# Kernel optimization log

Hardware: AMD Instinct MI355X
Metric: run time of the kernel (lower is better)

The kernel has to match this reference:

```python
import jax, jax.numpy as jnp
import numpy as np

NUM_HEADS = 16
HEAD_DIM = 128
HIDDEN = 2048
C_KV = 512
C_Q = 1024
ROPE_DIM = 64
BATCH = 2
SEQ = 2048
ROPE_BASE = 10000.0


def _rope_cos_sin(seq_len, dim, dtype):
    # standard RoPE tables: [seq, dim] with concatenated (half, half) freqs
    inv_freq = 1.0 / (ROPE_BASE ** (jnp.arange(0, dim, 2, dtype=jnp.float32) / dim))
    t = jnp.arange(seq_len, dtype=jnp.float32)
    freqs = jnp.outer(t, inv_freq)                      # [S, dim/2]
    emb = jnp.concatenate([freqs, freqs], axis=-1)      # [S, dim]
    return jnp.cos(emb).astype(dtype), jnp.sin(emb).astype(dtype)


def _rotate_half(x):
    x1, x2 = jnp.split(x, 2, axis=-1)
    return jnp.concatenate([-x2, x1], axis=-1)


def _apply_rope(x, cos, sin):
    # x: [B, S, H, D]; cos/sin: [S, D] -> broadcast over batch and heads
    c = cos[None, :, None, :]
    s = sin[None, :, None, :]
    return x * c + _rotate_half(x) * s


def setup_inputs() -> dict:
    key = jax.random.key(0)
    ks = jax.random.split(key, 10)

    def xavier(k, shape):
        fan_in, fan_out = shape
        limit = np.sqrt(6.0 / (fan_in + fan_out))
        return jax.random.uniform(k, shape, jnp.float32, -limit, limit)

    hidden_states = jax.random.normal(ks[0], (BATCH, SEQ, HIDDEN), jnp.float32)
    # causal mask: 1 = masked out (positions j > i)
    causal = jnp.triu(jnp.ones((SEQ, SEQ), jnp.int32), k=1)
    mask = jnp.broadcast_to(causal[None, None], (BATCH, 1, SEQ, SEQ))
    return {
        "hidden_states": hidden_states,
        "mask": mask,
        "W_DKV": xavier(ks[1], (HIDDEN, C_KV)),
        "W_UK": xavier(ks[2], (C_KV, NUM_HEADS * HEAD_DIM)),
        "W_UV": xavier(ks[3], (C_KV, NUM_HEADS * HEAD_DIM)),
        "W_DQ": xavier(ks[4], (HIDDEN, C_Q)),
        "W_UQ": xavier(ks[5], (C_Q, NUM_HEADS * HEAD_DIM)),
        "W_QR": xavier(ks[6], (C_Q, NUM_HEADS * ROPE_DIM)),
        "W_KR": xavier(ks[7], (HIDDEN, ROPE_DIM)),
        "W_O": xavier(ks[8], (NUM_HEADS * HEAD_DIM, HIDDEN)),
    }


def reference(hidden_states, mask, W_DKV, W_UK, W_UV, W_DQ, W_UQ, W_QR, W_KR, W_O):
    B, S, _ = hidden_states.shape
    scale = 1.0 / jnp.sqrt(jnp.float32(HEAD_DIM + ROPE_DIM))

    c_KV = hidden_states @ W_DKV                         # [B,S,c_kv]
    k_C = (c_KV @ W_UK).reshape(B, S, NUM_HEADS, HEAD_DIM)
    v = (c_KV @ W_UV).reshape(B, S, NUM_HEADS, HEAD_DIM)
    c_Q = hidden_states @ W_DQ                           # [B,S,c_q]
    q_C = (c_Q @ W_UQ).reshape(B, S, NUM_HEADS, HEAD_DIM)
    q_R = (c_Q @ W_QR).reshape(B, S, NUM_HEADS, ROPE_DIM)
    k_R = (hidden_states @ W_KR).reshape(B, S, 1, ROPE_DIM)

    cos, sin = _rope_cos_sin(S, ROPE_DIM, hidden_states.dtype)
    q_R = _apply_rope(q_R, cos, sin)
    k_R = _apply_rope(k_R, cos, sin)
    k_R = jnp.broadcast_to(k_R, (B, S, NUM_HEADS, ROPE_DIM))

    q = jnp.concatenate([q_C, q_R], axis=-1)             # [B,S,H,D+R]
    k = jnp.concatenate([k_C, k_R], axis=-1)             # [B,S,H,D+R]

    scores = jnp.einsum('bqhd,bkhd->bhqk', q, k) * scale
    scores = scores + mask.astype(scores.dtype) * jnp.asarray(-1e9, scores.dtype)
    probs = jax.nn.softmax(scores, axis=-1)
    out = jnp.einsum('bhqk,bkhd->bqhd', probs, v).reshape(B, S, NUM_HEADS * HEAD_DIM)
    return out @ W_O
```

## Files before the change

kernel.cpp:

```cpp
#include <hip/hip_runtime.h>
#include <hip/hip_bf16.h>

typedef __bf16 bf16x8 __attribute__((ext_vector_type(8)));
typedef float f32x4 __attribute__((ext_vector_type(4)));
typedef float f32x16 __attribute__((ext_vector_type(16)));
using BF = __hip_bfloat16;

constexpr int B_   = 2;
constexpr int S_   = 2048;
constexpr int NH_  = 16;
constexpr int HD_  = 128;
constexpr int HID_ = 2048;
constexpr int CKV_ = 512;
constexpr int CQ_  = 1024;
constexpr int RD_  = 64;
constexpr int M_   = B_ * S_;
constexpr int DQK_ = HD_ + RD_;

__device__ __forceinline__ f32x4 mfma16(bf16x8 a, bf16x8 b, f32x4 c) {
  return __builtin_amdgcn_mfma_f32_16x16x32_bf16(a, b, c, 0, 0, 0);
}
__device__ __forceinline__ f32x16 mfma32(bf16x8 a, bf16x8 b, f32x16 c) {
  return __builtin_amdgcn_mfma_f32_32x32x16_bf16(a, b, c, 0, 0, 0);
}
__device__ __forceinline__ unsigned cvtpk(float a, float b) {
  unsigned r;
  asm("v_cvt_pk_bf16_f32 %0, %1, %2" : "=v"(r) : "v"(a), "v"(b));
  return r;
}
__device__ __forceinline__ void gload16(const void* g, void* lds) {
  __builtin_amdgcn_global_load_lds((const __attribute__((address_space(1))) void*)g,
                                   (__attribute__((address_space(3))) void*)lds,
                                   16, 0, 0);
}
__device__ __forceinline__ void plswap(unsigned& x, unsigned& y, bool hi) {
#if __has_builtin(__builtin_amdgcn_permlane32_swap)
  typedef unsigned u32x2 __attribute__((ext_vector_type(2)));
  u32x2 r = __builtin_amdgcn_permlane32_swap(x, y, false, false);
  x = r[0];
  y = r[1];
#else
  unsigned sx = (unsigned)__shfl_xor((int)x, 32, 64);
  unsigned sy = (unsigned)__shfl_xor((int)y, 32, 64);
  unsigned nx = hi ? sy : x;
  unsigned ny = hi ? y : sx;
  x = nx;
  y = ny;
#endif
}

__global__ __launch_bounds__(256) void f2b_kern(const float* __restrict__ in,
                                                BF* __restrict__ out, int n4) {
  int i = blockIdx.x * 256 + threadIdx.x;
  if (i >= n4) return;
  float4 v = reinterpret_cast<const float4*>(in)[i];
  BF o[4] = {__float2bfloat16(v.x), __float2bfloat16(v.y),
             __float2bfloat16(v.z), __float2bfloat16(v.w)};
  reinterpret_cast<uint2*>(out)[i] = *reinterpret_cast<uint2*>(o);
}

__global__ __launch_bounds__(256) void wtrans_all(const float* __restrict__ w0,
                                                  const float* __restrict__ w1,
                                                  const float* __restrict__ w2,
                                                  const float* __restrict__ w3,
                                                  const float* __restrict__ w4,
                                                  const float* __restrict__ w5,
                                                  const float* __restrict__ w6,
                                                  const float* __restrict__ w7,
                                                  BF* __restrict__ tCat1,
                                                  BF* __restrict__ tCat2,
                                                  BF* __restrict__ tCat3,
                                                  BF* __restrict__ tWO) {
  const int cum[9] = {0, 1024, 3072, 3328, 4352, 5376, 7424, 8448, 12544};
  const int nxt[8] = {16, 32, 4, 64, 64, 64, 32, 64};
  const int Kt[8]  = {2048, 2048, 2048, 512, 512, 1024, 1024, 2048};
  const int Nt[8]  = {512, 1024, 64, 2048, 2048, 2048, 1024, 2048};
  int bid = blockIdx.x;
  int j = 0;
#pragma unroll
  for (int t = 1; t < 8; t++)
    if (bid >= cum[t]) j = t;
  const float* in = (j == 0) ? w0 : (j == 1) ? w1 : (j == 2) ? w2 : (j == 3) ? w3
                   : (j == 4) ? w4 : (j == 5) ? w5 : (j == 6) ? w6 : w7;
  BF* out = (j == 0) ? tCat1 : (j == 1) ? tCat1 + (size_t)512 * 2048
           : (j == 2) ? tCat1 + (size_t)1536 * 2048
           : (j == 3) ? tCat2 : (j == 4) ? tCat2 + (size_t)2048 * 512
           : (j == 5) ? tCat3 : (j == 6) ? tCat3 + (size_t)2048 * 1024 : tWO;
  const int K = Kt[j], N = Nt[j];
  int rem = bid - cum[j];
  int bx = rem % nxt[j], by = rem / nxt[j];
  int n0 = bx * 32, k0 = by * 32;

  __shared__ float t[32][33];
  int tx = threadIdx.x, ty = threadIdx.y;
#pragma unroll
  for (int j4 = 0; j4 < 4; j4++) {
    int k = k0 + ty + j4 * 8, n = n0 + tx;
    t[ty + j4 * 8][tx] = (n < N) ? in[(size_t)k * N + n] : 0.f;
  }
  __syncthreads();
#pragma unroll
  for (int j4 = 0; j4 < 4; j4++) {
    int n = n0 + ty + j4 * 8, k = k0 + tx;
    out[(size_t)n * K + k] = __float2bfloat16(t[tx][ty + j4 * 8]);
  }
}

template <int F>
__global__ __launch_bounds__(256) void gemm_f(const BF* __restrict__ A,
                                              const BF* __restrict__ Bt,
                                              void* __restrict__ C0,
                                              void* __restrict__ C1,
                                              void* __restrict__ C2,
                                              int M, int N, int K) {
  __shared__ BF As[3][128][32];
  __shared__ BF Bs[3][128][32];
  const int tid = threadIdx.x;
  const int w = tid >> 6, l = tid & 63;
  const int lr = l & 15, lg = l >> 4;
  const int wr = w >> 1, wc = w & 1;
  const int gx = gridDim.x;
  const int nwg = gx * gridDim.y;
  const int f = blockIdx.y * gx + blockIdx.x;
  const int swz = (f & 7) * (nwg >> 3) + (f >> 3);
  const int m0 = (swz / gx) * 128, n0 = (swz % gx) * 128;

  f32x4 acc[4][4];
#pragma unroll
  for (int m = 0; m < 4; m++)
#pragma unroll
    for (int n = 0; n < 4; n++) acc[m][n] = (f32x4){0.f, 0.f, 0.f, 0.f};

  auto STAGE = [&](int buf, int k0) {
#pragma unroll
    for (int j = 0; j < 2; j++) {
      int idx = tid + j * 256;
      int row = idx >> 2, seg = idx & 3;
      gload16(A + (size_t)(m0 + row) * K + k0 + seg * 8, &As[buf][0][0] + idx * 8);
      gload16(Bt + (size_t)(n0 + row) * K + k0 + seg * 8, &Bs[buf][0][0] + idx * 8);
    }
  };

  const int nk = K >> 5;
  STAGE(0, 0);
  if (nk > 1) STAGE(1, 32);
  asm volatile("s_waitcnt vmcnt(4)" ::: "memory");
  __builtin_amdgcn_sched_barrier(0);
  __builtin_amdgcn_s_barrier();

  int cur = 0;
  for (int ki = 0; ki < nk; ki++) {
    bf16x8 af[4], bfr[4];
#pragma unroll
    for (int m = 0; m < 4; m++)
      af[m] = *reinterpret_cast<const bf16x8*>(&As[cur][wr * 64 + m * 16 + lr][lg * 8]);
#pragma unroll
    for (int n = 0; n < 4; n++)
      bfr[n] = *reinterpret_cast<const bf16x8*>(&Bs[cur][wc * 64 + n * 16 + lr][lg * 8]);
    if (ki + 2 < nk) {
      int nb = cur + 2; if (nb >= 3) nb -= 3;
      STAGE(nb, (ki + 2) << 5);
    }
    __builtin_amdgcn_sched_barrier(0);
    __builtin_amdgcn_s_setprio(1);
#pragma unroll
    for (int m = 0; m < 4; m++)
#pragma unroll
      for (int n = 0; n < 4; n++) acc[m][n] = mfma16(af[m], bfr[n], acc[m][n]);
    __builtin_amdgcn_s_setprio(0);
    __builtin_amdgcn_sched_barrier(0);
    if (ki + 1 < nk) {
      if (ki + 2 < nk) {
        asm volatile("s_waitcnt vmcnt(4)" ::: "memory");
      } else {
        asm volatile("s_waitcnt vmcnt(0)" ::: "memory");
      }
      __builtin_amdgcn_sched_barrier(0);
      __builtin_amdgcn_s_barrier();
    }
    cur = cur + 1; if (cur >= 3) cur = 0;
  }

#pragma unroll
  for (int m = 0; m < 4; m++) {
#pragma unroll
    for (int n = 0; n < 4; n++) {
#pragma unroll
      for (int j = 0; j < 4; j++) {
        int row = m0 + wr * 64 + m * 16 + lg * 4 + j;
        int col = n0 + wc * 64 + n * 16 + lr;
        float v = acc[m][n][j];
        if constexpr (F == 1) {
          if (col < 512)
            ((BF*)C0)[(size_t)row * 512 + col] = __float2bfloat16(v);
          else if (col < 1536)
            ((BF*)C1)[(size_t)row * 1024 + (col - 512)] = __float2bfloat16(v);
          else
            ((BF*)C2)[(size_t)row * 128 + (col - 1536)] = __float2bfloat16(v);
        } else {
          ((float*)C0)[(size_t)row * 2048 + col] = v;
        }
      }
    }
  }
}

__global__ __launch_bounds__(256) void gemm_f23(const BF* __restrict__ cQ,
                                                const BF* __restrict__ t3,
                                                BF* __restrict__ qbuf,
                                                BF* __restrict__ qRt,
                                                const BF* __restrict__ cKV,
                                                const BF* __restrict__ t2,
                                                BF* __restrict__ kbuf,
                                                BF* __restrict__ vTb) {
  __shared__ BF As[3][128][32];
  __shared__ BF Bs[3][128][32];
  const int tid = threadIdx.x;
  const int w = tid >> 6, l = tid & 63;
  const int lr = l & 15, lg = l >> 4;
  const int wr = w >> 1, wc = w & 1;
  const int f = blockIdx.y * 56 + blockIdx.x;
  const int swz = (f & 7) * (1792 >> 3) + (f >> 3);
  const int xt = swz % 56;
  const int m0 = (swz / 56) * 128;
  const bool isF3 = xt < 24;
  const BF* A  = isF3 ? cQ : cKV;
  const BF* Bt = isF3 ? t3 : t2;
  const int K  = isF3 ? 1024 : 512;
  const int n0 = (isF3 ? xt : xt - 24) * 128;

  f32x4 acc[4][4];
#pragma unroll
  for (int m = 0; m < 4; m++)
#pragma unroll
    for (int n = 0; n < 4; n++) acc[m][n] = (f32x4){0.f, 0.f, 0.f, 0.f};

  auto STAGE = [&](int buf, int k0) {
#pragma unroll
    for (int j = 0; j < 2; j++) {
      int idx = tid + j * 256;
      int row = idx >> 2, seg = idx & 3;
      gload16(A + (size_t)(m0 + row) * K + k0 + seg * 8, &As[buf][0][0] + idx * 8);
      gload16(Bt + (size_t)(n0 + row) * K + k0 + seg * 8, &Bs[buf][0][0] + idx * 8);
    }
  };

  const int nk = K >> 5;
  STAGE(0, 0);
  STAGE(1, 32);
  asm volatile("s_waitcnt vmcnt(4)" ::: "memory");
  __builtin_amdgcn_sched_barrier(0);
  __builtin_amdgcn_s_barrier();

  int cur = 0;
  for (int ki = 0; ki < nk; ki++) {
    bf16x8 af[4], bfr[4];
#pragma unroll
    for (int m = 0; m < 4; m++)
      af[m] = *reinterpret_cast<const bf16x8*>(&As[cur][wr * 64 + m * 16 + lr][lg * 8]);
#pragma unroll
    for (int n = 0; n < 4; n++)
      bfr[n] = *reinterpret_cast<const bf16x8*>(&Bs[cur][wc * 64 + n * 16 + lr][lg * 8]);
    if (ki + 2 < nk) {
      int nb = cur + 2; if (nb >= 3) nb -= 3;
      STAGE(nb, (ki + 2) << 5);
    }
    __builtin_amdgcn_sched_barrier(0);
    __builtin_amdgcn_s_setprio(1);
#pragma unroll
    for (int m = 0; m < 4; m++)
#pragma unroll
      for (int n = 0; n < 4; n++) acc[m][n] = mfma16(af[m], bfr[n], acc[m][n]);
    __builtin_amdgcn_s_setprio(0);
    __builtin_amdgcn_sched_barrier(0);
    if (ki + 1 < nk) {
      if (ki + 2 < nk) {
        asm volatile("s_waitcnt vmcnt(4)" ::: "memory");
      } else {
        asm volatile("s_waitcnt vmcnt(0)" ::: "memory");
      }
      __builtin_amdgcn_sched_barrier(0);
      __builtin_amdgcn_s_barrier();
    }
    cur = cur + 1; if (cur >= 3) cur = 0;
  }

#pragma unroll
  for (int m = 0; m < 4; m++) {
#pragma unroll
    for (int n = 0; n < 4; n++) {
#pragma unroll
      for (int j = 0; j < 4; j++) {
        int row = m0 + wr * 64 + m * 16 + lg * 4 + j;
        int col = n0 + wc * 64 + n * 16 + lr;
        float v = acc[m][n][j];
        int b = row >> 11, s = row & 2047;
        if (isF3) {
          if (col < 2048) {
            int h = col >> 7, d = col & 127;
            qbuf[((size_t)(b * 16 + h) * 2048 + s) * 192 + d] = __float2bfloat16(v);
          } else {
            qRt[(size_t)row * 1024 + (col - 2048)] = __float2bfloat16(v);
          }
        } else {
          if (col < 2048) {
            int h = col >> 7, d = col & 127;
            kbuf[((size_t)(b * 16 + h) * 2048 + s) * 192 + d] = __float2bfloat16(v);
          } else {
            int c2 = col - 2048, h = c2 >> 7, d = c2 & 127;
            vTb[((size_t)(b * 16 + h) * 128 + d) * 2048 + s] = __float2bfloat16(v);
          }
        }
      }
    }
  }
}

__global__ __launch_bounds__(256) void rope_q(const BF* __restrict__ qr, BF* __restrict__ qb) {
  int idx = blockIdx.x * 256 + threadIdx.x;
  int d = idx & 63, h = (idx >> 6) & 15, m = idx >> 10;
  int s = m & 2047, b = m >> 11;
  float x = __bfloat162float(qr[(size_t)(m << 10) + (h << 6) + d]);
  float other = __bfloat162float(qr[(size_t)(m << 10) + (h << 6) + (d ^ 32)]);
  float rot = (d < 32) ? -other : other;
  int di = d & 31;
  float arg = (float)s * powf(10000.f, -(float)di / 32.0f);
  float c = cosf(arg), sn = sinf(arg);
  qb[((size_t)(b * 16 + h) * 2048 + s) * 192 + 128 + d] = __float2bfloat16(x * c + rot * sn);
}

__global__ __launch_bounds__(256) void rope_k(const BF* __restrict__ kr, BF* __restrict__ kb) {
  int idx = blockIdx.x * 256 + threadIdx.x;
  int d = idx & 63, m = idx >> 6;
  int s = m & 2047, b = m >> 11;
  float x = __bfloat162float(kr[(size_t)m * 128 + d]);
  float other = __bfloat162float(kr[(size_t)m * 128 + (d ^ 32)]);
  float rot = (d < 32) ? -other : other;
  int di = d & 31;
  float arg = (float)s * powf(10000.f, -(float)di / 32.0f);
  float val = x * cosf(arg) + rot * sinf(arg);
  BF v = __float2bfloat16(val);
#pragma unroll
  for (int h = 0; h < 16; h++)
    kb[((size_t)(b * 16 + h) * 2048 + s) * 192 + 128 + d] = v;
}

__global__ __launch_bounds__(256, 2) void attn_kern(const BF* __restrict__ qb,
                                                    const BF* __restrict__ kb,
                                                    const BF* __restrict__ vT,
                                                    BF* __restrict__ o) {
  const int yy = blockIdx.y;
  const bool second = yy >= 16;
  const int bh = second ? ((yy - 16) * 2 + 1) : (yy * 2);
  const int qt = second ? (int)blockIdx.x : (15 - (int)blockIdx.x);
  const int q0 = qt * 128;
  const int tid = threadIdx.x;
  const int w = tid >> 6, l = tid & 63;
  const int lo5 = l & 31;
  const int hi = l >> 5;
  const int l7 = l & 7;

  __shared__ __align__(16) char smem[81920];

  const int q = q0 + w * 32 + lo5;
  const int qmax = q0 + w * 32 + 31;

  bf16x8 aq[12];
  {
    const BF* qrow = qb + ((size_t)bh * 2048 + q) * 192;
#pragma unroll
    for (int kst = 0; kst < 12; kst++)
      aq[kst] = *reinterpret_cast<const bf16x8*>(qrow + kst * 16 + hi * 8);
  }

  f32x16 Oacc[4];
#pragma unroll
  for (int dt = 0; dt < 4; dt++)
#pragma unroll
    for (int r = 0; r < 16; r++) Oacc[dt][r] = 0.f;
  float mrow = -3e38f, lrow = 0.f;

  const float scale = 0.07216878364870323f;
  const int nch = (q0 + 128) >> 6;

  auto STAGE = [&](int buf, int ch) {
    const int cc = ch << 6;
    BF* Ks = (BF*)(smem + buf * 40960);
    BF* Vs = (BF*)(smem + buf * 40960 + 24576);
#pragma unroll
    for (int j2 = 0; j2 < 6; j2++) {
      int D = tid + j2 * 256;
      int row = D / 24, sp = D % 24;
      int sl = sp ^ (row & 7);
      gload16(kb + ((size_t)bh * 2048 + cc + row) * 192 + sl * 8, Ks + D * 8);
    }
#pragma unroll
    for (int j2 = 0; j2 < 4; j2++) {
      int D = tid + j2 * 256;
      int row = D >> 3, sp = D & 7;
      int sl = sp ^ (row & 7);
      gload16(vT + ((size_t)bh * 128 + row) * 2048 + cc + sl * 8, Vs + D * 8);
    }
  };

  STAGE(0, 0);
  __syncthreads();

  for (int ch = 0; ch < nch; ch++) {
    const int c0 = ch << 6;
    const int cur = ch & 1;
    if (ch + 1 < nch) STAGE(cur ^ 1, ch + 1);
    __builtin_amdgcn_sched_barrier(0);
    BF* Ks = (BF*)(smem + cur * 40960);
    BF* Vs = (BF*)(smem + cur * 40960 + 24576);

    f32x16 sf[2];
    __builtin_amdgcn_s_setprio(1);
#pragma unroll
    for (int t = 0; t < 2; t++) {
      if (c0 + t * 32 <= qmax) {
        f32x16 a0, a1;
#pragma unroll
        for (int r = 0; r < 16; r++) { a0[r] = 0.f; a1[r] = 0.f; }
#pragma unroll
        for (int kst = 0; kst < 12; kst++) {
          bf16x8 kfr = *reinterpret_cast<const bf16x8*>(
              Ks + (t * 32 + lo5) * 192 + (((kst * 2 + hi) ^ l7) * 8));
          if (kst & 1) a1 = mfma32(kfr, aq[kst], a1);
          else         a0 = mfma32(kfr, aq[kst], a0);
        }
        sf[t] = a0 + a1;
      } else {
#pragma unroll
        for (int r = 0; r < 16; r++) sf[t][r] = 0.f;
      }
    }
    __builtin_amdgcn_s_setprio(0);

    float mx = -3e38f;
#pragma unroll
    for (int t = 0; t < 2; t++) {
#pragma unroll
      for (int r = 0; r < 16; r++) {
        int key = c0 + t * 32 + (r & 3) + 8 * (r >> 2) + 4 * hi;
        float v = sf[t][r] * scale;
        v = (key <= q) ? v : -1e30f;
        sf[t][r] = v;
        mx = fmaxf(mx, v);
      }
    }
    mx = fmaxf(mx, __shfl_xor(mx, 32, 64));
    float mnew = fmaxf(mrow, mx);
    float corr = __expf(mrow - mnew);
    mrow = mnew;
    float psum = 0.f;
#pragma unroll
    for (int t = 0; t < 2; t++)
#pragma unroll
      for (int r = 0; r < 16; r++) {
        float p = __expf(sf[t][r] - mnew);
        sf[t][r] = p;
        psum += p;
      }
    psum += __shfl_xor(psum, 32, 64);
    lrow = lrow * corr + psum;
#pragma unroll
    for (int dt = 0; dt < 4; dt++) Oacc[dt] *= corr;

    bf16x8 pb[4];
#pragma unroll
    for (int ks = 0; ks < 4; ks++) {
      if (c0 + ks * 16 > qmax) continue;
      int t = ks >> 1, base = (ks & 1) * 8;
      unsigned Xa = cvtpk(sf[t][base + 0], sf[t][base + 1]);
      unsigned Xb = cvtpk(sf[t][base + 2], sf[t][base + 3]);
      unsigned Ya = cvtpk(sf[t][base + 4], sf[t][base + 5]);
      unsigned Yb = cvtpk(sf[t][base + 6], sf[t][base + 7]);
      plswap(Xa, Ya, hi != 0);
      plswap(Xb, Yb, hi != 0);
      union { unsigned u[4]; bf16x8 v; } pk_;
      pk_.u[0] = Xa; pk_.u[1] = Xb; pk_.u[2] = Ya; pk_.u[3] = Yb;
      pb[ks] = pk_.v;
    }

    __builtin_amdgcn_s_setprio(1);
#pragma unroll
    for (int ks = 0; ks < 4; ks++) {
      if (c0 + ks * 16 > qmax) continue;
#pragma unroll
      for (int dt = 0; dt < 4; dt++) {
        bf16x8 vfr = *reinterpret_cast<const bf16x8*>(
            Vs + (dt * 32 + lo5) * 64 + (((ks * 2 + hi) ^ l7) * 8));
        Oacc[dt] = mfma32(vfr, pb[ks], Oacc[dt]);
      }
    }
    __builtin_amdgcn_s_setprio(0);
    __syncthreads();
  }

  BF* Osh = (BF*)smem;
  float rinv = 1.0f / lrow;
  const int orow = w * 32 + lo5;
#pragma unroll
  for (int dt = 0; dt < 4; dt++) {
#pragma unroll
    for (int g = 0; g < 4; g++) {
      unsigned d0 = cvtpk(Oacc[dt][g * 4 + 0] * rinv, Oacc[dt][g * 4 + 1] * rinv);
      unsigned d1 = cvtpk(Oacc[dt][g * 4 + 2] * rinv, Oacc[dt][g * 4 + 3] * rinv);
      uint2 pr; pr.x = d0; pr.y = d1;
      *reinterpret_cast<uint2*>(Osh + orow * 136 + dt * 32 + g * 8 + hi * 4) = pr;
    }
  }
  __syncthreads();
  const int b = bh >> 4, h = bh & 15;
  const int cb = tid & 15, rb = tid >> 4;
#pragma unroll
  for (int rr = 0; rr < 8; rr++) {
    int row = rb + rr * 16;
    bf16x8 v = *reinterpret_cast<const bf16x8*>(Osh + row * 136 + cb * 8);
    *reinterpret_cast<bf16x8*>(o + ((size_t)(b * 2048 + q0 + row)) * 2048 + h * 128 + cb * 8) = v;
  }
}

extern "C" void kernel_launch(void* const* d_in, const int* in_sizes, int n_in,
                              void* d_out, int out_size, void* d_ws, size_t ws_size,
                              hipStream_t stream) {
  const float* hs   = (const float*)d_in[0];
  const float* wDKV = (const float*)d_in[2];
  const float* wUK  = (const float*)d_in[3];
  const float* wUV  = (const float*)d_in[4];
  const float* wDQ  = (const float*)d_in[5];
  const float* wUQ  = (const float*)d_in[6];
  const float* wQR  = (const float*)d_in[7];
  const float* wKR  = (const float*)d_in[8];
  const float* wO   = (const float*)d_in[9];
  float* out = (float*)d_out;

  char* ws = (char*)d_ws;
  size_t off = 0;
  auto alloc = [&](size_t bytes) -> char* {
    char* p = ws + off;
    off += (bytes + 255) & ~(size_t)255;
    return p;
  };
  BF* hsb   = (BF*)alloc((size_t)M_ * HID_ * 2);
  BF* tCat1 = (BF*)alloc((size_t)1664 * HID_ * 2);
  BF* tCat2 = (BF*)alloc((size_t)4096 * CKV_ * 2);
  BF* tCat3 = (BF*)alloc((size_t)3072 * CQ_ * 2);
  BF* tWO   = (BF*)alloc((size_t)HID_ * (NH_*HD_) * 2);
  BF* cKV   = (BF*)alloc((size_t)M_ * CKV_ * 2);
  BF* cQ    = (BF*)alloc((size_t)M_ * CQ_ * 2);
  BF* qbuf  = (BF*)alloc((size_t)B_ * NH_ * S_ * DQK_ * 2);
  BF* kbuf  = (BF*)alloc((size_t)B_ * NH_ * S_ * DQK_ * 2);
  BF* vTb   = (BF*)alloc((size_t)B_ * NH_ * HD_ * S_ * 2);
  BF* qRt   = (BF*)alloc((size_t)M_ * (NH_*RD_) * 2);
  BF* kRt   = (BF*)alloc((size_t)M_ * 128 * 2);
  BF* aout  = (BF*)alloc((size_t)M_ * (NH_*HD_) * 2);

  f2b_kern<<<(M_ * HID_ / 4 + 255) / 256, 256, 0, stream>>>(hs, hsb, M_ * HID_ / 4);

  wtrans_all<<<12544, dim3(32, 8), 0, stream>>>(wDKV, wDQ, wKR, wUK, wUV, wUQ, wQR, wO,
                                                tCat1, tCat2, tCat3, tWO);

  gemm_f<1><<<dim3(1664 / 128, M_ / 128), 256, 0, stream>>>(hsb, tCat1, cKV, cQ, kRt, M_, 1664, HID_);
  gemm_f23<<<dim3(56, M_ / 128), 256, 0, stream>>>(cQ, tCat3, qbuf, qRt, cKV, tCat2, kbuf, vTb);

  rope_q<<<(M_ * NH_ * RD_) / 256, 256, 0, stream>>>(qRt, qbuf);
  rope_k<<<(M_ * RD_) / 256, 256, 0, stream>>>(kRt, kbuf);

  attn_kern<<<dim3(S_ / 128, B_ * NH_), 256, 0, stream>>>(qbuf, kbuf, vTb, aout);

  gemm_f<4><<<dim3(2048 / 128, M_ / 128), 256, 0, stream>>>(aout, tWO, out, nullptr, nullptr, M_, 2048, HID_);
}
```

Baseline: 316.2 us.

## Stage gemm_f23 epilogue through LDS for vectorized stores; lazy softmax rescale

The gemm_f23 epilogue now writes the accumulator tile into shared memory, transposing it for the V output, then emits coalesced 16-byte stores to qbuf, qRt, kbuf and vTb. The old scalar scattered bf16 stores, and the strided transposed writes to vTb, are removed. Separately, the attention kernel skips the online-softmax rescale of O and l unless the running max grows by more than 8 anywhere in the wave. This saves exps and multiplies, but lets unnormalized exponents reach up to e^8, a small precision risk. The launch grid dimensions are rewritten as literals with the same values.

```diff
diff --git a/kernel.cpp b/kernel.cpp
--- a/kernel.cpp
+++ b/kernel.cpp
@@ -213,8 +213,9 @@
                                                 const BF* __restrict__ t2,
                                                 BF* __restrict__ kbuf,
                                                 BF* __restrict__ vTb) {
-  __shared__ BF As[3][128][32];
-  __shared__ BF Bs[3][128][32];
+  __shared__ BF sm[3 * 128 * 32 * 2];
+  BF* Asm = sm;
+  BF* Bsm = sm + 3 * 128 * 32;
   const int tid = threadIdx.x;
   const int w = tid >> 6, l = tid & 63;
   const int lr = l & 15, lg = l >> 4;
@@ -240,8 +241,8 @@
     for (int j = 0; j < 2; j++) {
       int idx = tid + j * 256;
       int row = idx >> 2, seg = idx & 3;
-      gload16(A + (size_t)(m0 + row) * K + k0 + seg * 8, &As[buf][0][0] + idx * 8);
-      gload16(Bt + (size_t)(n0 + row) * K + k0 + seg * 8, &Bs[buf][0][0] + idx * 8);
+      gload16(A + (size_t)(m0 + row) * K + k0 + seg * 8, Asm + buf * 4096 + idx * 8);
+      gload16(Bt + (size_t)(n0 + row) * K + k0 + seg * 8, Bsm + buf * 4096 + idx * 8);
     }
   };
 
@@ -257,10 +258,10 @@
     bf16x8 af[4], bfr[4];
 #pragma unroll
     for (int m = 0; m < 4; m++)
-      af[m] = *reinterpret_cast<const bf16x8*>(&As[cur][wr * 64 + m * 16 + lr][lg * 8]);
+      af[m] = *reinterpret_cast<const bf16x8*>(Asm + cur * 4096 + (wr * 64 + m * 16 + lr) * 32 + lg * 8);
 #pragma unroll
     for (int n = 0; n < 4; n++)
-      bfr[n] = *reinterpret_cast<const bf16x8*>(&Bs[cur][wc * 64 + n * 16 + lr][lg * 8]);
+      bfr[n] = *reinterpret_cast<const bf16x8*>(Bsm + cur * 4096 + (wc * 64 + n * 16 + lr) * 32 + lg * 8);
     if (ki + 2 < nk) {
       int nb = cur + 2; if (nb >= 3) nb -= 3;
       STAGE(nb, (ki + 2) << 5);
@@ -285,32 +286,59 @@
     cur = cur + 1; if (cur >= 3) cur = 0;
   }
 
+  const bool TR = (!isF3) && (n0 >= 2048);
+  __syncthreads();
+  BF* Cs = sm;
 #pragma unroll
   for (int m = 0; m < 4; m++) {
 #pragma unroll
     for (int n = 0; n < 4; n++) {
 #pragma unroll
       for (int j = 0; j < 4; j++) {
-        int row = m0 + wr * 64 + m * 16 + lg * 4 + j;
-        int col = n0 + wc * 64 + n * 16 + lr;
-        float v = acc[m][n][j];
-        int b = row >> 11, s = row & 2047;
-        if (isF3) {
-          if (col < 2048) {
-            int h = col >> 7, d = col & 127;
-            qbuf[((size_t)(b * 16 + h) * 2048 + s) * 192 + d] = __float2bfloat16(v);
-          } else {
-            qRt[(size_t)row * 1024 + (col - 2048)] = __float2bfloat16(v);
-          }
-        } else {
-          if (col < 2048) {
-            int h = col >> 7, d = col & 127;
-            kbuf[((size_t)(b * 16 + h) * 2048 + s) * 192 + d] = __float2bfloat16(v);
-          } else {
-            int c2 = col - 2048, h = c2 >> 7, d = c2 & 127;
-            vTb[((size_t)(b * 16 + h) * 128 + d) * 2048 + s] = __float2bfloat16(v);
-          }
-        }
+        int r = wr * 64 + m * 16 + lg * 4 + j;
+        int c = wc * 64 + n * 16 + lr;
+        BF v = __float2bfloat16(acc[m][n][j]);
+        if (TR) Cs[c * 132 + r] = v;
+        else    Cs[r * 132 + c] = v;
+      }
+    }
+  }
+  __syncthreads();
+  const int cb = tid & 15, rb = tid >> 4;
+  const int b = m0 >> 11, s0 = m0 & 2047;
+  if (isF3) {
+    if (n0 < 2048) {
+      int h = n0 >> 7;
+#pragma unroll
+      for (int pass = 0; pass < 8; pass++) {
+        int r = rb + pass * 16;
+        bf16x8 v = *reinterpret_cast<const bf16x8*>(&Cs[r * 132 + cb * 8]);
+        *reinterpret_cast<bf16x8*>(qbuf + ((size_t)(b * 16 + h) * 2048 + s0 + r) * 192 + cb * 8) = v;
+      }
+    } else {
+#pragma unroll
+      for (int pass = 0; pass < 8; pass++) {
+        int r = rb + pass * 16;
+        bf16x8 v = *reinterpret_cast<const bf16x8*>(&Cs[r * 132 + cb * 8]);
+        *reinterpret_cast<bf16x8*>(qRt + (size_t)(m0 + r) * 1024 + (n0 - 2048) + cb * 8) = v;
+      }
+    }
+  } else {
+    if (n0 < 2048) {
+      int h = n0 >> 7;
+#pragma unroll
+      for (int pass = 0; pass < 8; pass++) {
+        int r = rb + pass * 16;
+        bf16x8 v = *reinterpret_cast<const bf16x8*>(&Cs[r * 132 + cb * 8]);
+        *reinterpret_cast<bf16x8*>(kbuf + ((size_t)(b * 16 + h) * 2048 + s0 + r) * 192 + cb * 8) = v;
+      }
+    } else {
+      int h = (n0 - 2048) >> 7;
+#pragma unroll
+      for (int pass = 0; pass < 8; pass++) {
+        int d = rb + pass * 16;
+        bf16x8 v = *reinterpret_cast<const bf16x8*>(&Cs[d * 132 + cb * 8]);
+        *reinterpret_cast<bf16x8*>(vTb + ((size_t)(b * 16 + h) * 128 + d) * 2048 + s0 + cb * 8) = v;
       }
     }
   }
@@ -450,22 +478,25 @@
       }
     }
     mx = fmaxf(mx, __shfl_xor(mx, 32, 64));
-    float mnew = fmaxf(mrow, mx);
-    float corr = __expf(mrow - mnew);
-    mrow = mnew;
+    if (!__all(mx - mrow <= 8.0f)) {
+      float mnew = fmaxf(mrow, mx);
+      float corr = __expf(mrow - mnew);
+      mrow = mnew;
+      lrow *= corr;
+#pragma unroll
+      for (int dt = 0; dt < 4; dt++) Oacc[dt] *= corr;
+    }
     float psum = 0.f;
 #pragma unroll
     for (int t = 0; t < 2; t++)
 #pragma unroll
       for (int r = 0; r < 16; r++) {
-        float p = __expf(sf[t][r] - mnew);
+        float p = __expf(sf[t][r] - mrow);
         sf[t][r] = p;
         psum += p;
       }
     psum += __shfl_xor(psum, 32, 64);
-    lrow = lrow * corr + psum;
-#pragma unroll
-    for (int dt = 0; dt < 4; dt++) Oacc[dt] *= corr;
+    lrow += psum;
 
     bf16x8 pb[4];
 #pragma unroll
@@ -562,13 +593,13 @@
   wtrans_all<<<12544, dim3(32, 8), 0, stream>>>(wDKV, wDQ, wKR, wUK, wUV, wUQ, wQR, wO,
                                                 tCat1, tCat2, tCat3, tWO);
 
-  gemm_f<1><<<dim3(1664 / 128, M_ / 128), 256, 0, stream>>>(hsb, tCat1, cKV, cQ, kRt, M_, 1664, HID_);
-  gemm_f23<<<dim3(56, M_ / 128), 256, 0, stream>>>(cQ, tCat3, qbuf, qRt, cKV, tCat2, kbuf, vTb);
+  gemm_f<1><<<dim3(13, 32), 256, 0, stream>>>(hsb, tCat1, cKV, cQ, kRt, M_, 1664, HID_);
+  gemm_f23<<<dim3(56, 32), 256, 0, stream>>>(cQ, tCat3, qbuf, qRt, cKV, tCat2, kbuf, vTb);
 
   rope_q<<<(M_ * NH_ * RD_) / 256, 256, 0, stream>>>(qRt, qbuf);
   rope_k<<<(M_ * RD_) / 256, 256, 0, stream>>>(kRt, kbuf);
 
   attn_kern<<<dim3(S_ / 128, B_ * NH_), 256, 0, stream>>>(qbuf, kbuf, vTb, aout);
 
-  gemm_f<4><<<dim3(2048 / 128, M_ / 128), 256, 0, stream>>>(aout, tWO, out, nullptr, nullptr, M_, 2048, HID_);
-}
+  gemm_f<4><<<dim3(16, 32), 256, 0, stream>>>(aout, tWO, out, nullptr, nullptr, M_, 2048, HID_);
+}
```

Result: faster. 286.4 us (-9.4%).
